# Performance work log

Hardware: AMD Instinct MI355X
Metric: run time of the kernel (lower is better)

The kernel has to match this reference:

```python
import jax, jax.numpy as jnp
import numpy as np

TAU = 2.0
ALPHA = 4.0  # spikingjelly surrogate.Sigmoid default
NUM_HEADS = 8


def lif(x, v_th):
    # Multi-step LIF over leading time axis T. v_reset=0, hard reset, tau=2.
    # Forward: Heaviside spike; backward: sigmoid surrogate via straight-through.
    def step(v, xt):
        v = v + (xt - v) / TAU
        hard = (v >= v_th).astype(xt.dtype)
        soft = jax.nn.sigmoid(ALPHA * (v - v_th))
        spike = soft + jax.lax.stop_gradient(hard - soft)
        v = v * (1.0 - jax.lax.stop_gradient(hard))  # detach_reset hard reset to 0
        return v, spike
    _, out = jax.lax.scan(step, jnp.zeros_like(x[0]), x)
    return out


def conv_bn_lif(x, w, scale, bias, v_th=1.0):
    # 1x1 conv (no bias) + folded eval-mode BatchNorm + LIF.
    # x: [T,B,C,H,W], w: [Cout,Cin], scale/bias: [Cout]
    y = jnp.einsum('tbchw,dc->tbdhw', x, w)
    y = y * scale[:, None, None] + bias[:, None, None]
    return lif(y, v_th)


def setup_inputs() -> dict:
    key = jax.random.key(0)
    ks = jax.random.split(key, 14)
    T, B, C, H, W = 4, 32, 384, 14, 14
    x = jax.random.normal(ks[0], (T, B, C, H, W), dtype=jnp.float32)
    def conv_params(k):
        k1, k2, k3 = jax.random.split(k, 3)
        w = jax.random.normal(k1, (C, C), dtype=jnp.float32) * (1.0 / np.sqrt(C))
        scale = jax.random.uniform(k2, (C,), dtype=jnp.float32, minval=0.5, maxval=1.5)
        bias = jax.random.normal(k3, (C,), dtype=jnp.float32) * 0.1
        return w, scale, bias
    wq, sq, bq = conv_params(ks[1])
    wk, sk, bk = conv_params(ks[2])
    wv, sv, bv = conv_params(ks[3])
    wp, sp, bp = conv_params(ks[4])
    return {"x": x, "wq": wq, "sq": sq, "bq": bq, "wk": wk, "sk": sk, "bk": bk,
            "wv": wv, "sv": sv, "bv": bv, "wp": wp, "sp": sp, "bp": bp}


def reference(x, wq, sq, bq, wk, sk, bk, wv, sv, bv, wp, sp, bp):
    T, B, C, H, W = x.shape
    h = NUM_HEADS
    d = C // h
    N = H * W
    # QKV: conv+BN+LIF -> binary spikes [T,B,C,H,W]
    qs = conv_bn_lif(x, wq, sq, bq)
    ks_ = conv_bn_lif(x, wk, sk, bk)
    vs = conv_bn_lif(x, wv, sv, bv)
    # [T,B,C,H,W] -> [T,B,h,d,N] -> [T,B,h,N,d]
    def to_heads(t):
        return t.reshape(T, B, h, d, N).transpose(0, 1, 2, 4, 3)
    q, k, v = to_heads(qs), to_heads(ks_), to_heads(vs)
    attn = jnp.einsum('tbhnd,tbhmd->tbhnm', q, k)
    out = jnp.einsum('tbhnm,tbhmd->tbhnd', attn, v) * 0.125
    out = lif(out, 0.5)  # attn_lif v_threshold=0.5
    # [T,B,h,N,d] -> [T,B,h,d,N] -> [T,B,C,H,W]
    out = out.transpose(0, 1, 2, 4, 3).reshape(T, B, C, H, W)
    out = conv_bn_lif(out, wp, sp, bp)
    return out
```

## Files before the change

kernel.cpp:

```cpp
#include <hip/hip_runtime.h>


#define T_ 4
#define B_ 32
#define C_ 384
#define N_ 196
#define NH_ 8
#define D_ 48
#define TB_ (T_ * B_)
#define CN_ ((size_t)C_ * N_)
#define BCN4_ (B_ * C_ * (N_ / 4))
#define TBCN_ ((size_t)T_ * B_ * C_ * N_)
typedef unsigned long long u64;

__global__ __launch_bounds__(256, 2) void gemm_f32(
    const float* __restrict__ X, const float* __restrict__ W0,
    const float* __restrict__ W1, const float* __restrict__ W2,
    float* __restrict__ P)
{
  const int g = blockIdx.z;
  const float* __restrict__ W = (g == 0) ? W0 : (g == 1) ? W1 : W2;
  const int co0 = blockIdx.y * 128;
  const int j0 = blockIdx.x * 128;
  __shared__ float As[16][128];
  __shared__ float Bs[16][128];
  const int tid = threadIdx.x;
  const int tx = tid & 15, ty = tid >> 4;

  const int bcol = (tid & 31) * 4;
  const int bk = tid >> 5;
  const int bj = j0 + bcol;
  const int btb = bj / N_;
  const float* xb = X + (size_t)btb * CN_ + (bj - btb * N_);
  const int arow = tid >> 1;
  const int ac8 = (tid & 1) * 8;

  float acc[8][8] = {};
  for (int c0 = 0; c0 < C_; c0 += 16) {
    const float* wrow = W + (size_t)(co0 + arow) * C_ + c0 + ac8;
    const float4 a0 = *(const float4*)wrow;
    const float4 a1 = *(const float4*)(wrow + 4);
    As[ac8 + 0][arow] = a0.x; As[ac8 + 1][arow] = a0.y;
    As[ac8 + 2][arow] = a0.z; As[ac8 + 3][arow] = a0.w;
    As[ac8 + 4][arow] = a1.x; As[ac8 + 5][arow] = a1.y;
    As[ac8 + 6][arow] = a1.z; As[ac8 + 7][arow] = a1.w;
    *(float4*)&Bs[bk][bcol]     = *(const float4*)(xb + (size_t)(c0 + bk) * N_);
    *(float4*)&Bs[bk + 8][bcol] = *(const float4*)(xb + (size_t)(c0 + bk + 8) * N_);
    __syncthreads();
#pragma unroll
    for (int k = 0; k < 16; ++k) {
      float a[8], b[8];
      *(float4*)&a[0] = *(const float4*)&As[k][ty * 4];
      *(float4*)&a[4] = *(const float4*)&As[k][64 + ty * 4];
      *(float4*)&b[0] = *(const float4*)&Bs[k][tx * 4];
      *(float4*)&b[4] = *(const float4*)&Bs[k][64 + tx * 4];
#pragma unroll
      for (int i = 0; i < 8; ++i)
#pragma unroll
        for (int j = 0; j < 8; ++j)
          acc[i][j] = fmaf(a[i], b[j], acc[i][j]);
    }
    __syncthreads();
  }
#pragma unroll
  for (int cg = 0; cg < 2; ++cg) {
    const int jj = j0 + cg * 64 + tx * 4;
    const int tb = jj / N_;
    float* pb = P + (size_t)(g * TB_ + tb) * CN_ + (jj - tb * N_);
#pragma unroll
    for (int rg = 0; rg < 2; ++rg) {
#pragma unroll
      for (int i = 0; i < 4; ++i) {
        const int r = rg * 4 + i;
        const int co = co0 + rg * 64 + ty * 4 + i;
        *(float4*)&pb[(size_t)co * N_] = make_float4(
            acc[r][cg * 4 + 0], acc[r][cg * 4 + 1],
            acc[r][cg * 4 + 2], acc[r][cg * 4 + 3]);
      }
    }
  }
}

__global__ __launch_bounds__(256) void lif4(
    const float* __restrict__ In, float* __restrict__ Out,
    const float* __restrict__ s0, const float* __restrict__ b0, float vth)
{
  const long u = (long)blockIdx.x * 256 + threadIdx.x;
  if (u >= BCN4_) return;
  const long r = u;
  const int c = (int)((r / (N_ / 4)) % C_);
  const bool has_bn = (s0 != nullptr);
  const float sc = has_bn ? s0[c] : 1.0f;
  const float bi = has_bn ? b0[c] : 0.0f;
  const float4* In4 = (const float4*)In;
  float4* Out4 = (float4*)Out;
  float v[4] = {0.f, 0.f, 0.f, 0.f};
#pragma unroll
  for (int t = 0; t < T_; ++t) {
    const long idx = (long)t * BCN4_ + r;
    const float4 y4 = In4[idx];
    float y[4] = {y4.x, y4.y, y4.z, y4.w};
    float o[4];
#pragma unroll
    for (int e = 0; e < 4; ++e) {
      const float yb = has_bn ? __fadd_rn(__fmul_rn(y[e], sc), bi) : y[e];
      v[e] = __fadd_rn(v[e], __fmul_rn(__fsub_rn(yb, v[e]), 0.5f));
      const bool fire = (v[e] >= vth);
      o[e] = fire ? 1.0f : 0.0f;
      v[e] = fire ? 0.0f : v[e];
    }
    Out4[idx] = make_float4(o[0], o[1], o[2], o[3]);
  }
}

__global__ __launch_bounds__(1024) void fused_attn(
    const float* __restrict__ P, float* __restrict__ O,
    const float* __restrict__ sq, const float* __restrict__ bq,
    const float* __restrict__ sk, const float* __restrict__ bk,
    const float* __restrict__ sv, const float* __restrict__ bv)
{
  const int h = blockIdx.x;
  const int b = blockIdx.y;
  __shared__ u64 msk[3][T_][D_][4];
  __shared__ u64 qT[T_][208];
  __shared__ u64 Gp[T_][8][D_];
  const int tid = threadIdx.x;
  const int wave = tid >> 6, lane = tid & 63;

  for (int task = wave; task < 3 * D_ * 4; task += 16) {
    const int g = task / (D_ * 4);
    const int rem = task - g * (D_ * 4);
    const int j = rem >> 2, w = rem & 3;
    const int m = w * 64 + lane;
    const bool act = (m < N_);
    const int mc = act ? m : (N_ - 1);
    const int c = h * D_ + j;
    const float sc = (g == 0 ? sq : g == 1 ? sk : sv)[c];
    const float bi = (g == 0 ? bq : g == 1 ? bk : bv)[c];
    const float* base = P + (size_t)g * TB_ * CN_ + (size_t)b * CN_
                          + (size_t)c * N_ + mc;
    float y[T_];
#pragma unroll
    for (int t = 0; t < T_; ++t) y[t] = base[(size_t)t * B_ * CN_];
    float v = 0.f;
#pragma unroll
    for (int t = 0; t < T_; ++t) {
      const float yb = __fadd_rn(__fmul_rn(y[t], sc), bi);
      v = __fadd_rn(v, __fmul_rn(__fsub_rn(yb, v), 0.5f));
      const bool fire = (v >= 1.0f);
      if (fire) v = 0.f;
      const u64 bl = __ballot(fire && act);
      if (lane == 0) msk[g][t][j][w] = bl;
    }
  }
  __syncthreads();

  {
    const int t = wave >> 2, w = wave & 3;
    const int n = w * 64 + lane;
    u64 qr = 0ull;
#pragma unroll 8
    for (int j = 0; j < D_; ++j)
      qr |= ((msk[0][t][j][w] >> lane) & 1ull) << j;
    if (n < N_) qT[t][n] = qr;
  }
  for (int task = wave; task < T_ * D_; task += 16) {
    const int t = task / D_, d = task - (task / D_) * D_;
    const bool ja = (lane < D_);
    const int j = ja ? lane : (D_ - 1);
    const u64* kj = msk[1][t][j];
    const u64* vd = msk[2][t][d];
    const int gi = __popcll(kj[0] & vd[0]) + __popcll(kj[1] & vd[1]) +
                   __popcll(kj[2] & vd[2]) + __popcll(kj[3] & vd[3]);
#pragma unroll
    for (int p = 0; p < 8; ++p) {
      const u64 bl = __ballot(ja && ((gi >> p) & 1));
      if (lane == 0) Gp[t][p][d] = bl;
    }
  }
  __syncthreads();

  const int u = tid;
  if (u < 4 * N_) {
    const int dq = u / N_;
    const int n = u - dq * N_;
    const int d0 = dq * 12;
    float vmem[12];
#pragma unroll
    for (int i = 0; i < 12; ++i) vmem[i] = 0.f;
    for (int t = 0; t < T_; ++t) {
      const u64 qr = qT[t][n];
      float* ob = O + ((size_t)(t * B_ + b) * C_ + h * D_ + d0) * N_ + n;
#pragma unroll
      for (int i = 0; i < 12; ++i) {
        int acc = 0;
#pragma unroll
        for (int p = 0; p < 8; ++p)
          acc += __popcll(qr & Gp[t][p][d0 + i]) << p;
        const float y = __int2float_rn(acc) * 0.125f;
        vmem[i] = __fadd_rn(vmem[i], __fmul_rn(__fsub_rn(y, vmem[i]), 0.5f));
        const bool fire = (vmem[i] >= 0.5f);
        ob[(size_t)i * N_] = fire ? 1.0f : 0.0f;
        if (fire) vmem[i] = 0.f;
      }
    }
  }
}

extern "C" void kernel_launch(void* const* d_in, const int* in_sizes, int n_in,
                              void* d_out, int out_size, void* d_ws, size_t ws_size,
                              hipStream_t stream) {
  const float* x  = (const float*)d_in[0];
  const float* wq = (const float*)d_in[1];
  const float* sq = (const float*)d_in[2];
  const float* bq = (const float*)d_in[3];
  const float* wk = (const float*)d_in[4];
  const float* sk = (const float*)d_in[5];
  const float* bk = (const float*)d_in[6];
  const float* wv = (const float*)d_in[7];
  const float* sv = (const float*)d_in[8];
  const float* bv = (const float*)d_in[9];
  const float* wp = (const float*)d_in[10];
  const float* sp = (const float*)d_in[11];
  const float* bp = (const float*)d_in[12];
  float* out = (float*)d_out;

  float* P = (float*)d_ws;
  float* O = P + 3 * TBCN_;
  float* P2 = P;

  gemm_f32<<<dim3(196, 3, 3), 256, 0, stream>>>(x, wq, wk, wv, P);
  fused_attn<<<dim3(NH_, B_), 1024, 0, stream>>>(P, O, sq, bq, sk, bk, sv, bv);
  gemm_f32<<<dim3(196, 3, 1), 256, 0, stream>>>(O, wp, wp, wp, P2);
  lif4<<<dim3((BCN4_ + 255) / 256), 256, 0, stream>>>(P2, out, sp, bp, 1.0f);
}
```

Measured before the change: 536.4 us.

## Retile GEMM to 96x512 blocks of 768 threads and batch attention mask loads

The 1x1-conv GEMM now uses 768-thread blocks covering 96 output channels by 512 columns, so each block reuses the weight tile across a much wider column strip and loads of X are shared across more output rows. Each wave now computes 8 rows by 8 columns split into two 256-column halves, and stores are coalesced along columns. The attention kernel's spike-mask stage now issues the global loads for four tasks before computing any of them, to expose more memory-level parallelism. The bigger tile raises LDS and register use per block and changes the grid to fewer, larger blocks, which may lower occupancy.

```diff
diff --git a/kernel.cpp b/kernel.cpp
--- a/kernel.cpp
+++ b/kernel.cpp
@@ -13,47 +13,47 @@
 #define TBCN_ ((size_t)T_ * B_ * C_ * N_)
 typedef unsigned long long u64;
 
-__global__ __launch_bounds__(256, 2) void gemm_f32(
+__global__ __launch_bounds__(768, 3) void gemm_bw(
     const float* __restrict__ X, const float* __restrict__ W0,
     const float* __restrict__ W1, const float* __restrict__ W2,
     float* __restrict__ P)
 {
   const int g = blockIdx.z;
   const float* __restrict__ W = (g == 0) ? W0 : (g == 1) ? W1 : W2;
-  const int co0 = blockIdx.y * 128;
-  const int j0 = blockIdx.x * 128;
-  __shared__ float As[16][128];
-  __shared__ float Bs[16][128];
+  const int co0 = blockIdx.y * 96;
+  const int j0 = blockIdx.x * 512;
+  __shared__ float Bs[16][512];
+  __shared__ float As[16][100];
   const int tid = threadIdx.x;
-  const int tx = tid & 15, ty = tid >> 4;
-
-  const int bcol = (tid & 31) * 4;
-  const int bk = tid >> 5;
-  const int bj = j0 + bcol;
-  const int btb = bj / N_;
-  const float* xb = X + (size_t)btb * CN_ + (bj - btb * N_);
-  const int arow = tid >> 1;
-  const int ac8 = (tid & 1) * 8;
-
+  const int wave = tid >> 6, lane = tid & 63;
+  const int w8 = wave * 8;
+  const int lane4 = lane * 4;
+
+  const int ar = tid >> 2, aq = tid & 3;
   float acc[8][8] = {};
+
   for (int c0 = 0; c0 < C_; c0 += 16) {
-    const float* wrow = W + (size_t)(co0 + arow) * C_ + c0 + ac8;
-    const float4 a0 = *(const float4*)wrow;
-    const float4 a1 = *(const float4*)(wrow + 4);
-    As[ac8 + 0][arow] = a0.x; As[ac8 + 1][arow] = a0.y;
-    As[ac8 + 2][arow] = a0.z; As[ac8 + 3][arow] = a0.w;
-    As[ac8 + 4][arow] = a1.x; As[ac8 + 5][arow] = a1.y;
-    As[ac8 + 6][arow] = a1.z; As[ac8 + 7][arow] = a1.w;
-    *(float4*)&Bs[bk][bcol]     = *(const float4*)(xb + (size_t)(c0 + bk) * N_);
-    *(float4*)&Bs[bk + 8][bcol] = *(const float4*)(xb + (size_t)(c0 + bk + 8) * N_);
+    if (tid < 384) {
+      const float4 w4 = *(const float4*)(W + (size_t)(co0 + ar) * C_ + c0 + aq * 4);
+      As[aq * 4 + 0][ar] = w4.x; As[aq * 4 + 1][ar] = w4.y;
+      As[aq * 4 + 2][ar] = w4.z; As[aq * 4 + 3][ar] = w4.w;
+    }
+    for (int u = tid; u < 2048; u += 768) {
+      const int k = u >> 7;
+      const int colq = (u & 127) * 4;
+      const int j = j0 + colq;
+      const int tb = j / N_;
+      *(float4*)&Bs[k][colq] =
+          *(const float4*)(X + (size_t)tb * CN_ + (size_t)(c0 + k) * N_ + (j - tb * N_));
+    }
     __syncthreads();
 #pragma unroll
     for (int k = 0; k < 16; ++k) {
       float a[8], b[8];
-      *(float4*)&a[0] = *(const float4*)&As[k][ty * 4];
-      *(float4*)&a[4] = *(const float4*)&As[k][64 + ty * 4];
-      *(float4*)&b[0] = *(const float4*)&Bs[k][tx * 4];
-      *(float4*)&b[4] = *(const float4*)&Bs[k][64 + tx * 4];
+      *(float4*)&a[0] = *(const float4*)&As[k][w8];
+      *(float4*)&a[4] = *(const float4*)&As[k][w8 + 4];
+      *(float4*)&b[0] = *(const float4*)&Bs[k][lane4];
+      *(float4*)&b[4] = *(const float4*)&Bs[k][256 + lane4];
 #pragma unroll
       for (int i = 0; i < 8; ++i)
 #pragma unroll
@@ -62,21 +62,17 @@
     }
     __syncthreads();
   }
-#pragma unroll
-  for (int cg = 0; cg < 2; ++cg) {
-    const int jj = j0 + cg * 64 + tx * 4;
-    const int tb = jj / N_;
-    float* pb = P + (size_t)(g * TB_ + tb) * CN_ + (jj - tb * N_);
-#pragma unroll
-    for (int rg = 0; rg < 2; ++rg) {
-#pragma unroll
-      for (int i = 0; i < 4; ++i) {
-        const int r = rg * 4 + i;
-        const int co = co0 + rg * 64 + ty * 4 + i;
-        *(float4*)&pb[(size_t)co * N_] = make_float4(
-            acc[r][cg * 4 + 0], acc[r][cg * 4 + 1],
-            acc[r][cg * 4 + 2], acc[r][cg * 4 + 3]);
-      }
+  {
+    const int jA = j0 + lane4;
+    const int jB = j0 + 256 + lane4;
+    const int tbA = jA / N_, tbB = jB / N_;
+    float* pA = P + (size_t)(g * TB_ + tbA) * CN_ + (jA - tbA * N_);
+    float* pB = P + (size_t)(g * TB_ + tbB) * CN_ + (jB - tbB * N_);
+#pragma unroll
+    for (int i = 0; i < 8; ++i) {
+      const size_t ro = (size_t)(co0 + w8 + i) * N_;
+      *(float4*)&pA[ro] = make_float4(acc[i][0], acc[i][1], acc[i][2], acc[i][3]);
+      *(float4*)&pB[ro] = make_float4(acc[i][4], acc[i][5], acc[i][6], acc[i][7]);
     }
   }
 }
@@ -127,30 +123,41 @@
   const int tid = threadIdx.x;
   const int wave = tid >> 6, lane = tid & 63;
 
-  for (int task = wave; task < 3 * D_ * 4; task += 16) {
-    const int g = task / (D_ * 4);
-    const int rem = task - g * (D_ * 4);
-    const int j = rem >> 2, w = rem & 3;
-    const int m = w * 64 + lane;
-    const bool act = (m < N_);
-    const int mc = act ? m : (N_ - 1);
-    const int c = h * D_ + j;
-    const float sc = (g == 0 ? sq : g == 1 ? sk : sv)[c];
-    const float bi = (g == 0 ? bq : g == 1 ? bk : bv)[c];
-    const float* base = P + (size_t)g * TB_ * CN_ + (size_t)b * CN_
-                          + (size_t)c * N_ + mc;
-    float y[T_];
-#pragma unroll
-    for (int t = 0; t < T_; ++t) y[t] = base[(size_t)t * B_ * CN_];
-    float v = 0.f;
-#pragma unroll
-    for (int t = 0; t < T_; ++t) {
-      const float yb = __fadd_rn(__fmul_rn(y[t], sc), bi);
-      v = __fadd_rn(v, __fmul_rn(__fsub_rn(yb, v), 0.5f));
-      const bool fire = (v >= 1.0f);
-      if (fire) v = 0.f;
-      const u64 bl = __ballot(fire && act);
-      if (lane == 0) msk[g][t][j][w] = bl;
+  for (int base = wave; base < 3 * D_ * 4; base += 64) {
+    float y[4][T_];
+    float sc[4], bi[4];
+    int gj[4], jj[4], ww[4];
+    bool act[4];
+#pragma unroll
+    for (int q = 0; q < 4; ++q) {
+      const int task = base + q * 16;
+      const int g = task / (D_ * 4);
+      const int rem = task - g * (D_ * 4);
+      const int j = rem >> 2, w = rem & 3;
+      gj[q] = g; jj[q] = j; ww[q] = w;
+      const int m = w * 64 + lane;
+      act[q] = (m < N_);
+      const int mc = act[q] ? m : (N_ - 1);
+      const int c = h * D_ + j;
+      sc[q] = (g == 0 ? sq : g == 1 ? sk : sv)[c];
+      bi[q] = (g == 0 ? bq : g == 1 ? bk : bv)[c];
+      const float* bp_ = P + (size_t)g * TB_ * CN_ + (size_t)b * CN_
+                           + (size_t)c * N_ + mc;
+#pragma unroll
+      for (int t = 0; t < T_; ++t) y[q][t] = bp_[(size_t)t * B_ * CN_];
+    }
+#pragma unroll
+    for (int q = 0; q < 4; ++q) {
+      float v = 0.f;
+#pragma unroll
+      for (int t = 0; t < T_; ++t) {
+        const float yb = __fadd_rn(__fmul_rn(y[q][t], sc[q]), bi[q]);
+        v = __fadd_rn(v, __fmul_rn(__fsub_rn(yb, v), 0.5f));
+        const bool fire = (v >= 1.0f);
+        if (fire) v = 0.f;
+        const u64 bl = __ballot(fire && act[q]);
+        if (lane == 0) msk[gj[q]][t][jj[q]][ww[q]] = bl;
+      }
     }
   }
   __syncthreads();
@@ -229,8 +236,8 @@
   float* O = P + 3 * TBCN_;
   float* P2 = P;
 
-  gemm_f32<<<dim3(196, 3, 3), 256, 0, stream>>>(x, wq, wk, wv, P);
+  gemm_bw<<<dim3(49, 4, 3), 768, 0, stream>>>(x, wq, wk, wv, P);
   fused_attn<<<dim3(NH_, B_), 1024, 0, stream>>>(P, O, sq, bq, sk, bk, sv, bv);
-  gemm_f32<<<dim3(196, 3, 1), 256, 0, stream>>>(O, wp, wp, wp, P2);
+  gemm_bw<<<dim3(49, 4, 1), 768, 0, stream>>>(O, wp, wp, wp, P2);
   lif4<<<dim3((BCN4_ + 255) / 256), 256, 0, stream>>>(P2, out, sp, bp, 1.0f);
 }
```

Result: slower. 608.4 us (+13.4%).

## Split spike-mask generation into wide kernel and retile GEMM to 128x256 blocks

Applied to the files above, without the earlier changes.

The mask/LIF stage that read the QKV projections is moved out of the 256-block attention kernel into a separate kernel with 9216 blocks. Each wave handles one channel across all positions and writes ballot bitmasks to a global buffer, which the attention kernel then copies into shared memory. This spreads the memory-bound read of the QKV outputs across far more blocks, at the cost of an extra launch and a global round-trip for the masks. The GEMM is also retiled to 512 threads over 128x256 tiles with 16x4 per-thread outputs and a padded A tile in shared memory, changing register use and occupancy.

```diff
diff --git a/kernel.cpp b/kernel.cpp
--- a/kernel.cpp
+++ b/kernel.cpp
@@ -13,7 +13,7 @@
 #define TBCN_ ((size_t)T_ * B_ * C_ * N_)
 typedef unsigned long long u64;
 
-__global__ __launch_bounds__(256, 2) void gemm_f32(
+__global__ __launch_bounds__(512) void gemm_f32(
     const float* __restrict__ X, const float* __restrict__ W0,
     const float* __restrict__ W1, const float* __restrict__ W2,
     float* __restrict__ P)
@@ -21,64 +21,50 @@
   const int g = blockIdx.z;
   const float* __restrict__ W = (g == 0) ? W0 : (g == 1) ? W1 : W2;
   const int co0 = blockIdx.y * 128;
-  const int j0 = blockIdx.x * 128;
-  __shared__ float As[16][128];
-  __shared__ float Bs[16][128];
+  const int j0 = blockIdx.x * 256;
+  __shared__ float As[16][132];
+  __shared__ float Bs[16][256];
   const int tid = threadIdx.x;
-  const int tx = tid & 15, ty = tid >> 4;
-
-  const int bcol = (tid & 31) * 4;
-  const int bk = tid >> 5;
-  const int bj = j0 + bcol;
+  const int wave = tid >> 6, lane = tid & 63;
+  const int w16 = wave * 16;
+  const int lane4 = lane * 4;
+
+  const int ar = tid >> 2, aq4 = (tid & 3) * 4;
+  const float* wrow = W + (size_t)(co0 + ar) * C_ + aq4;
+  const int bj = j0 + lane4;
   const int btb = bj / N_;
-  const float* xb = X + (size_t)btb * CN_ + (bj - btb * N_);
-  const int arow = tid >> 1;
-  const int ac8 = (tid & 1) * 8;
-
-  float acc[8][8] = {};
+  const float* xcol = X + (size_t)btb * CN_ + (bj - btb * N_);
+  float* pbase = P + (size_t)(g * TB_ + btb) * CN_ + (bj - btb * N_);
+
+  float acc[16][4] = {};
   for (int c0 = 0; c0 < C_; c0 += 16) {
-    const float* wrow = W + (size_t)(co0 + arow) * C_ + c0 + ac8;
-    const float4 a0 = *(const float4*)wrow;
-    const float4 a1 = *(const float4*)(wrow + 4);
-    As[ac8 + 0][arow] = a0.x; As[ac8 + 1][arow] = a0.y;
-    As[ac8 + 2][arow] = a0.z; As[ac8 + 3][arow] = a0.w;
-    As[ac8 + 4][arow] = a1.x; As[ac8 + 5][arow] = a1.y;
-    As[ac8 + 6][arow] = a1.z; As[ac8 + 7][arow] = a1.w;
-    *(float4*)&Bs[bk][bcol]     = *(const float4*)(xb + (size_t)(c0 + bk) * N_);
-    *(float4*)&Bs[bk + 8][bcol] = *(const float4*)(xb + (size_t)(c0 + bk + 8) * N_);
+    const float4 w4 = *(const float4*)(wrow + c0);
+    As[aq4 + 0][ar] = w4.x; As[aq4 + 1][ar] = w4.y;
+    As[aq4 + 2][ar] = w4.z; As[aq4 + 3][ar] = w4.w;
+    *(float4*)&Bs[wave][lane4] =
+        *(const float4*)(xcol + (size_t)(c0 + wave) * N_);
+    *(float4*)&Bs[wave + 8][lane4] =
+        *(const float4*)(xcol + (size_t)(c0 + wave + 8) * N_);
     __syncthreads();
 #pragma unroll
     for (int k = 0; k < 16; ++k) {
-      float a[8], b[8];
-      *(float4*)&a[0] = *(const float4*)&As[k][ty * 4];
-      *(float4*)&a[4] = *(const float4*)&As[k][64 + ty * 4];
-      *(float4*)&b[0] = *(const float4*)&Bs[k][tx * 4];
-      *(float4*)&b[4] = *(const float4*)&Bs[k][64 + tx * 4];
-#pragma unroll
-      for (int i = 0; i < 8; ++i)
-#pragma unroll
-        for (int j = 0; j < 8; ++j)
-          acc[i][j] = fmaf(a[i], b[j], acc[i][j]);
+      float b[4], a[16];
+      *(float4*)&b[0] = *(const float4*)&Bs[k][lane4];
+#pragma unroll
+      for (int q = 0; q < 4; ++q)
+        *(float4*)&a[q * 4] = *(const float4*)&As[k][w16 + q * 4];
+#pragma unroll
+      for (int i = 0; i < 16; ++i)
+#pragma unroll
+        for (int jj = 0; jj < 4; ++jj)
+          acc[i][jj] = fmaf(a[i], b[jj], acc[i][jj]);
     }
     __syncthreads();
   }
 #pragma unroll
-  for (int cg = 0; cg < 2; ++cg) {
-    const int jj = j0 + cg * 64 + tx * 4;
-    const int tb = jj / N_;
-    float* pb = P + (size_t)(g * TB_ + tb) * CN_ + (jj - tb * N_);
-#pragma unroll
-    for (int rg = 0; rg < 2; ++rg) {
-#pragma unroll
-      for (int i = 0; i < 4; ++i) {
-        const int r = rg * 4 + i;
-        const int co = co0 + rg * 64 + ty * 4 + i;
-        *(float4*)&pb[(size_t)co * N_] = make_float4(
-            acc[r][cg * 4 + 0], acc[r][cg * 4 + 1],
-            acc[r][cg * 4 + 2], acc[r][cg * 4 + 3]);
-      }
-    }
-  }
+  for (int i = 0; i < 16; ++i)
+    *(float4*)&pbase[(size_t)(co0 + w16 + i) * N_] =
+        make_float4(acc[i][0], acc[i][1], acc[i][2], acc[i][3]);
 }
 
 __global__ __launch_bounds__(256) void lif4(
@@ -113,11 +99,53 @@
   }
 }
 
-__global__ __launch_bounds__(1024) void fused_attn(
-    const float* __restrict__ P, float* __restrict__ O,
+__global__ __launch_bounds__(256) void k_mask(
+    const float* __restrict__ P, u64* __restrict__ MSK,
     const float* __restrict__ sq, const float* __restrict__ bq,
     const float* __restrict__ sk, const float* __restrict__ bk,
     const float* __restrict__ sv, const float* __restrict__ bv)
+{
+  const int wave = threadIdx.x >> 6, lane = threadIdx.x & 63;
+  const int task = blockIdx.x * 4 + wave;
+  const int j = task % D_;
+  int r = task / D_;
+  const int b = r & 31; r >>= 5;
+  const int h = r & 7;  r >>= 3;
+  const int g = r;
+  const int c = h * D_ + j;
+  const float sc = (g == 0 ? sq : g == 1 ? sk : sv)[c];
+  const float bi = (g == 0 ? bq : g == 1 ? bk : bv)[c];
+  const float* base = P + (size_t)g * TB_ * CN_ + (size_t)b * CN_ + (size_t)c * N_;
+
+  float y[4][T_];
+  bool act[4];
+#pragma unroll
+  for (int w = 0; w < 4; ++w) {
+    const int m = w * 64 + lane;
+    act[w] = (m < N_);
+    const int mc = act[w] ? m : (N_ - 1);
+#pragma unroll
+    for (int t = 0; t < T_; ++t)
+      y[w][t] = base[(size_t)t * B_ * CN_ + mc];
+  }
+  u64* mb = MSK + ((size_t)(h * 32 + b) * 3 + g) * (T_ * D_ * 4) + j * 4;
+  float v[4] = {0.f, 0.f, 0.f, 0.f};
+#pragma unroll
+  for (int t = 0; t < T_; ++t) {
+#pragma unroll
+    for (int w = 0; w < 4; ++w) {
+      const float yb = __fadd_rn(__fmul_rn(y[w][t], sc), bi);
+      v[w] = __fadd_rn(v[w], __fmul_rn(__fsub_rn(yb, v[w]), 0.5f));
+      const bool fire = (v[w] >= 1.0f);
+      if (fire) v[w] = 0.f;
+      const u64 bl = __ballot(fire && act[w]);
+      if (lane == 0) mb[(size_t)t * (D_ * 4) + w] = bl;
+    }
+  }
+}
+
+__global__ __launch_bounds__(1024) void k_attn(
+    const u64* __restrict__ MSK, float* __restrict__ O)
 {
   const int h = blockIdx.x;
   const int b = blockIdx.y;
@@ -127,31 +155,10 @@
   const int tid = threadIdx.x;
   const int wave = tid >> 6, lane = tid & 63;
 
-  for (int task = wave; task < 3 * D_ * 4; task += 16) {
-    const int g = task / (D_ * 4);
-    const int rem = task - g * (D_ * 4);
-    const int j = rem >> 2, w = rem & 3;
-    const int m = w * 64 + lane;
-    const bool act = (m < N_);
-    const int mc = act ? m : (N_ - 1);
-    const int c = h * D_ + j;
-    const float sc = (g == 0 ? sq : g == 1 ? sk : sv)[c];
-    const float bi = (g == 0 ? bq : g == 1 ? bk : bv)[c];
-    const float* base = P + (size_t)g * TB_ * CN_ + (size_t)b * CN_
-                          + (size_t)c * N_ + mc;
-    float y[T_];
-#pragma unroll
-    for (int t = 0; t < T_; ++t) y[t] = base[(size_t)t * B_ * CN_];
-    float v = 0.f;
-#pragma unroll
-    for (int t = 0; t < T_; ++t) {
-      const float yb = __fadd_rn(__fmul_rn(y[t], sc), bi);
-      v = __fadd_rn(v, __fmul_rn(__fsub_rn(yb, v), 0.5f));
-      const bool fire = (v >= 1.0f);
-      if (fire) v = 0.f;
-      const u64 bl = __ballot(fire && act);
-      if (lane == 0) msk[g][t][j][w] = bl;
-    }
+  {
+    const u64* ms = MSK + (size_t)(h * 32 + b) * 2304;
+    u64* mf = &msk[0][0][0][0];
+    for (int off = tid; off < 2304; off += 1024) mf[off] = ms[off];
   }
   __syncthreads();
 
@@ -227,10 +234,12 @@
 
   float* P = (float*)d_ws;
   float* O = P + 3 * TBCN_;
+  u64* MSK = (u64*)(P + 4 * TBCN_);
   float* P2 = P;
 
-  gemm_f32<<<dim3(196, 3, 3), 256, 0, stream>>>(x, wq, wk, wv, P);
-  fused_attn<<<dim3(NH_, B_), 1024, 0, stream>>>(P, O, sq, bq, sk, bk, sv, bv);
-  gemm_f32<<<dim3(196, 3, 1), 256, 0, stream>>>(O, wp, wp, wp, P2);
+  gemm_f32<<<dim3(98, 3, 3), 512, 0, stream>>>(x, wq, wk, wv, P);
+  k_mask<<<dim3(9216), 256, 0, stream>>>(P, MSK, sq, bq, sk, bk, sv, bv);
+  k_attn<<<dim3(NH_, B_), 1024, 0, stream>>>(MSK, O);
+  gemm_f32<<<dim3(98, 3, 1), 512, 0, stream>>>(O, wp, wp, wp, P2);
   lif4<<<dim3((BCN4_ + 255) / 256), 256, 0, stream>>>(P2, out, sp, bp, 1.0f);
 }
```

Measured after the change: 575.8 us. 1.07x slower.

## Split spike-mask generation out of fused attention into a highly parallel kernel

Applied to the files above, without the earlier changes.

Moves the QKV BN+LIF bitmask construction out of the 256-block attention kernel into a separate kernel with 9216 blocks, one wave per channel row. The masks go to a global workspace and the attention kernel loads them into shared memory. This raises memory-level parallelism for the large P reads. The cost is an extra launch, a small global mask round-trip, and reliance on extra workspace space.

```diff
diff --git a/kernel.cpp b/kernel.cpp
--- a/kernel.cpp
+++ b/kernel.cpp
@@ -113,11 +113,53 @@
   }
 }
 
-__global__ __launch_bounds__(1024) void fused_attn(
-    const float* __restrict__ P, float* __restrict__ O,
+__global__ __launch_bounds__(256) void k_mask(
+    const float* __restrict__ P, u64* __restrict__ MSK,
     const float* __restrict__ sq, const float* __restrict__ bq,
     const float* __restrict__ sk, const float* __restrict__ bk,
     const float* __restrict__ sv, const float* __restrict__ bv)
+{
+  const int wave = threadIdx.x >> 6, lane = threadIdx.x & 63;
+  const int task = blockIdx.x * 4 + wave;
+  const int j = task % D_;
+  int r = task / D_;
+  const int b = r & 31; r >>= 5;
+  const int h = r & 7;  r >>= 3;
+  const int g = r;
+  const int c = h * D_ + j;
+  const float sc = (g == 0 ? sq : g == 1 ? sk : sv)[c];
+  const float bi = (g == 0 ? bq : g == 1 ? bk : bv)[c];
+  const float* base = P + (size_t)g * TB_ * CN_ + (size_t)b * CN_ + (size_t)c * N_;
+
+  float y[4][T_];
+  bool act[4];
+#pragma unroll
+  for (int w = 0; w < 4; ++w) {
+    const int m = w * 64 + lane;
+    act[w] = (m < N_);
+    const int mc = act[w] ? m : (N_ - 1);
+#pragma unroll
+    for (int t = 0; t < T_; ++t)
+      y[w][t] = base[(size_t)t * B_ * CN_ + mc];
+  }
+  u64* mb = MSK + ((size_t)(h * 32 + b) * 3 + g) * (T_ * D_ * 4) + j * 4;
+  float v[4] = {0.f, 0.f, 0.f, 0.f};
+#pragma unroll
+  for (int t = 0; t < T_; ++t) {
+#pragma unroll
+    for (int w = 0; w < 4; ++w) {
+      const float yb = __fadd_rn(__fmul_rn(y[w][t], sc), bi);
+      v[w] = __fadd_rn(v[w], __fmul_rn(__fsub_rn(yb, v[w]), 0.5f));
+      const bool fire = (v[w] >= 1.0f);
+      if (fire) v[w] = 0.f;
+      const u64 bl = __ballot(fire && act[w]);
+      if (lane == 0) mb[(size_t)t * (D_ * 4) + w] = bl;
+    }
+  }
+}
+
+__global__ __launch_bounds__(1024) void k_attn(
+    const u64* __restrict__ MSK, float* __restrict__ O)
 {
   const int h = blockIdx.x;
   const int b = blockIdx.y;
@@ -127,31 +169,10 @@
   const int tid = threadIdx.x;
   const int wave = tid >> 6, lane = tid & 63;
 
-  for (int task = wave; task < 3 * D_ * 4; task += 16) {
-    const int g = task / (D_ * 4);
-    const int rem = task - g * (D_ * 4);
-    const int j = rem >> 2, w = rem & 3;
-    const int m = w * 64 + lane;
-    const bool act = (m < N_);
-    const int mc = act ? m : (N_ - 1);
-    const int c = h * D_ + j;
-    const float sc = (g == 0 ? sq : g == 1 ? sk : sv)[c];
-    const float bi = (g == 0 ? bq : g == 1 ? bk : bv)[c];
-    const float* base = P + (size_t)g * TB_ * CN_ + (size_t)b * CN_
-                          + (size_t)c * N_ + mc;
-    float y[T_];
-#pragma unroll
-    for (int t = 0; t < T_; ++t) y[t] = base[(size_t)t * B_ * CN_];
-    float v = 0.f;
-#pragma unroll
-    for (int t = 0; t < T_; ++t) {
-      const float yb = __fadd_rn(__fmul_rn(y[t], sc), bi);
-      v = __fadd_rn(v, __fmul_rn(__fsub_rn(yb, v), 0.5f));
-      const bool fire = (v >= 1.0f);
-      if (fire) v = 0.f;
-      const u64 bl = __ballot(fire && act);
-      if (lane == 0) msk[g][t][j][w] = bl;
-    }
+  {
+    const u64* ms = MSK + (size_t)(h * 32 + b) * 2304;
+    u64* mf = &msk[0][0][0][0];
+    for (int off = tid; off < 2304; off += 1024) mf[off] = ms[off];
   }
   __syncthreads();
 
@@ -227,10 +248,12 @@
 
   float* P = (float*)d_ws;
   float* O = P + 3 * TBCN_;
+  u64* MSK = (u64*)(P + 4 * TBCN_);
   float* P2 = P;
 
   gemm_f32<<<dim3(196, 3, 3), 256, 0, stream>>>(x, wq, wk, wv, P);
-  fused_attn<<<dim3(NH_, B_), 1024, 0, stream>>>(P, O, sq, bq, sk, bk, sv, bv);
+  k_mask<<<dim3(9216), 256, 0, stream>>>(P, MSK, sq, bq, sk, bk, sv, bv);
+  k_attn<<<dim3(NH_, B_), 1024, 0, stream>>>(MSK, O);
   gemm_f32<<<dim3(196, 3, 1), 256, 0, stream>>>(O, wp, wp, wp, P2);
   lif4<<<dim3((BCN4_ + 255) / 256), 256, 0, stream>>>(P2, out, sp, bp, 1.0f);
 }
```

Result: faster. 505.9 us (-5.7%).
